# Performance work log

Hardware: AMD Instinct MI355X
Metric: run time of the kernel (lower is better)

Reference implementation:

```python
import jax, jax.numpy as jnp
import numpy as np

N = 8192
CUTOFF_LOWER = 0.0
CUTOFF_UPPER = 5.0
MAX_PAIRS = 64 * N  # max_num_pairs = -64 -> 64 neighbors per atom
BOX_L = 45.0


def setup_inputs() -> dict:
    key = jax.random.key(0)
    k1, _ = jax.random.split(key)
    pos = jax.random.uniform(k1, (N, 3), dtype=jnp.float32) * BOX_L
    batch = jnp.zeros((N,), dtype=jnp.int32)
    return {"pos": pos, "batch": batch}


def reference(pos, batch):
    # Brute O(N^2) neighbor search, cutoff_lower <= r < cutoff_upper,
    # loop=False (no self pairs), include_transpose=True (both (i,j) and (j,i)),
    # resize_to_fit=False: fixed-size output padded with (-1,-1) pairs.
    n = pos.shape[0]
    diff = pos[:, None, :] - pos[None, :, :]          # [N, N, 3] edge_vec = pos_i - pos_j
    d2 = jnp.sum(diff * diff, axis=-1)                 # [N, N]
    same_batch = batch[:, None] == batch[None, :]
    not_self = ~jnp.eye(n, dtype=bool)
    mask = same_batch & not_self & (d2 < CUTOFF_UPPER ** 2) & (d2 >= CUTOFF_LOWER ** 2)
    flat = mask.reshape(-1)
    count = jnp.sum(flat)
    # static-size compaction (jit-compatible): first MAX_PAIRS hits in row-major order
    idx = jnp.nonzero(flat, size=MAX_PAIRS, fill_value=0)[0]
    valid = jnp.arange(MAX_PAIRS) < jnp.minimum(count, MAX_PAIRS)
    i = idx // n
    j = idx % n
    edge_vec = jnp.where(valid[:, None], diff.reshape(n * n, 3)[idx], 0.0)
    d2_g = d2.reshape(-1)[idx]
    edge_weight = jnp.where(valid, jnp.sqrt(jnp.where(valid, d2_g, 1.0)), 0.0)
    edge_index = jnp.stack([jnp.where(valid, i, -1), jnp.where(valid, j, -1)], axis=0)
    edge_index = edge_index.astype(jnp.int64) if jax.config.jax_enable_x64 else edge_index.astype(jnp.int32)
    return edge_index, edge_weight, edge_vec
```

## Files before the change

### kernel.cpp

```cpp
#include <hip/hip_runtime.h>

#define NATOMS 8192
#define MAXP (64 * NATOMS)
#define R2CUT 25.0f

constexpr int ROWW = 128;
constexpr int NC1 = 9;
constexpr int NCELL = NC1 * NC1 * NC1;

__device__ __forceinline__ float d2_exact(float dx, float dy, float dz) {
    return __fadd_rn(__fadd_rn(__fmul_rn(dx, dx), __fmul_rn(dy, dy)),
                     __fmul_rn(dz, dz));
}

__device__ __forceinline__ int cellOf(float v) {
    int c = (int)((double)v * 0.2);
    return c < 0 ? 0 : (c > NC1 - 1 ? NC1 - 1 : c);
}

__global__ __launch_bounds__(256) void nl_init(float4* __restrict__ out) {
    const int total4 = 6 * MAXP / 4;
    const int neg4   = 2 * MAXP / 4;
    const float4 negv  = make_float4(-1.f, -1.f, -1.f, -1.f);
    const float4 zerov = make_float4(0.f, 0.f, 0.f, 0.f);
    int idx = blockIdx.x * blockDim.x + threadIdx.x;
    int stride = gridDim.x * blockDim.x;
    for (int k = idx; k < total4; k += stride)
        out[k] = (k < neg4) ? negv : zerov;
}

__global__ __launch_bounds__(1024) void bin_all(const float* __restrict__ pos,
                                                int* __restrict__ cellStart,
                                                int* __restrict__ sortedIdx,
                                                float4* __restrict__ sortedPos) {
    __shared__ unsigned int hist[NCELL];
    __shared__ unsigned int scanbuf[1024];
    __shared__ unsigned int starts[NCELL + 1];
    const int t = threadIdx.x;
    if (t < NCELL) hist[t] = 0u;
    __syncthreads();
    int myCell[8], mySlot[8];
#pragma unroll
    for (int k = 0; k < 8; ++k) {
        const int a = t + k * 1024;
        const float x = pos[3 * a], y = pos[3 * a + 1], z = pos[3 * a + 2];
        const int c = (cellOf(z) * NC1 + cellOf(y)) * NC1 + cellOf(x);
        myCell[k] = c;
        mySlot[k] = (int)atomicAdd(&hist[c], 1u);
    }
    __syncthreads();
    const unsigned int v = (t < NCELL) ? hist[t] : 0u;
    scanbuf[t] = v;
    __syncthreads();
    for (int off = 1; off < 1024; off <<= 1) {
        const unsigned int u = (t >= off) ? scanbuf[t - off] : 0u;
        __syncthreads();
        scanbuf[t] += u;
        __syncthreads();
    }
    const unsigned int ex = scanbuf[t] - v;
    if (t < NCELL) { starts[t] = ex; cellStart[t] = (int)ex; }
    if (t == 0)    { starts[NCELL] = NATOMS; cellStart[NCELL] = NATOMS; }
    __syncthreads();
#pragma unroll
    for (int k = 0; k < 8; ++k) {
        const int a = t + k * 1024;
        const int p = (int)starts[myCell[k]] + mySlot[k];
        sortedIdx[p] = a;
        sortedPos[p] = make_float4(pos[3 * a], pos[3 * a + 1], pos[3 * a + 2], 0.f);
    }
}

__global__ __launch_bounds__(512) void nl_neigh(const float* __restrict__ pos,
                                                const int* __restrict__ batch,
                                                const int* __restrict__ cellStart,
                                                const int* __restrict__ sortedIdx,
                                                const float4* __restrict__ sortedPos,
                                                unsigned short* __restrict__ rowbuf,
                                                int* __restrict__ counts) {
    __shared__ unsigned int bm[8][256];
    const int tid = threadIdx.x;
    const int lane = tid & 63;
    const int wave = tid >> 6;
    const int i = blockIdx.x * 8 + wave;
    unsigned int* sb = bm[wave];
    sb[lane] = 0u; sb[lane + 64] = 0u; sb[lane + 128] = 0u; sb[lane + 192] = 0u;

    const float xi = pos[3 * i], yi = pos[3 * i + 1], zi = pos[3 * i + 2];
    const int bi = batch[i];
    const int cx = cellOf(xi), cy = cellOf(yi), cz = cellOf(zi);
    const int xlo = cx > 0 ? cx - 1 : 0;
    const int xhi = cx < NC1 - 1 ? cx + 1 : NC1 - 1;

    for (int dz = -1; dz <= 1; ++dz) {
        const int czz = cz + dz;
        if ((unsigned)czz > (unsigned)(NC1 - 1)) continue;
        for (int dy = -1; dy <= 1; ++dy) {
            const int cyy = cy + dy;
            if ((unsigned)cyy > (unsigned)(NC1 - 1)) continue;
            const int base = (czz * NC1 + cyy) * NC1;
            const int s = cellStart[base + xlo];
            const int e = cellStart[base + xhi + 1];
            for (int k = s + lane; k < e; k += 64) {
                const float4 p = sortedPos[k];
                const int j = sortedIdx[k];
                const float dxv = xi - p.x;
                const float dyv = yi - p.y;
                const float dzv = zi - p.z;
                const float d2 = d2_exact(dxv, dyv, dzv);
                if (d2 < R2CUT && j != i && batch[j] == bi)
                    atomicOr(&sb[j >> 5], 1u << (j & 31));
            }
        }
    }

    unsigned short* rb = rowbuf + (size_t)i * ROWW;
    int total = 0;
#pragma unroll
    for (int g = 0; g < 4; ++g) {
        unsigned int w = sb[g * 64 + lane];
        const int c = __popc(w);
        int incl = c;
        for (int off = 1; off < 64; off <<= 1) {
            const int u = __shfl_up(incl, off);
            if (lane >= off) incl += u;
        }
        int o = total + incl - c;
        const unsigned int jbase = (unsigned)(g * 64 + lane) * 32u;
        while (w) {
            const int b = __ffs(w) - 1;
            w &= w - 1u;
            if (o < ROWW) rb[o] = (unsigned short)(jbase + (unsigned)b);
            ++o;
        }
        total += __shfl(incl, 63);
    }
    if (lane == 0) counts[i] = total > ROWW ? ROWW : total;
}

__global__ __launch_bounds__(256) void nl_scan(const int* __restrict__ counts,
                                               int* __restrict__ offsets) {
    __shared__ int ssum[256];
    const int tid = threadIdx.x;
    const int base = tid * 32;
    int c[32];
    int s = 0;
#pragma unroll
    for (int k = 0; k < 32; ++k) { c[k] = counts[base + k]; s += c[k]; }
    ssum[tid] = s;
    __syncthreads();
    for (int off = 1; off < 256; off <<= 1) {
        const int v = (tid >= off) ? ssum[tid - off] : 0;
        __syncthreads();
        ssum[tid] += v;
        __syncthreads();
    }
    int run = ssum[tid] - s;
#pragma unroll
    for (int k = 0; k < 32; ++k) { offsets[base + k] = run; run += c[k]; }
}

__global__ __launch_bounds__(512) void nl_scatter(const float* __restrict__ pos,
                                                  const unsigned short* __restrict__ rowbuf,
                                                  const int* __restrict__ counts,
                                                  const int* __restrict__ offsets,
                                                  float* __restrict__ out) {
    const int tid = threadIdx.x;
    const int lane = tid & 63;
    const int wave = tid >> 6;
    const int i = blockIdx.x * 8 + wave;
    const int cnt = counts[i];
    const int base = offsets[i];
    const float xi = pos[3 * i], yi = pos[3 * i + 1], zi = pos[3 * i + 2];
    const float fi = (float)i;
    const unsigned short* rb = rowbuf + (size_t)i * ROWW;
    float* __restrict__ outI = out;
    float* __restrict__ outJ = out + MAXP;
    float* __restrict__ outW = out + 2 * MAXP;
    float* __restrict__ outV = out + 3 * MAXP;
    for (int k = lane; k < cnt; k += 64) {
        const int j = rb[k];
        const float dxv = xi - pos[3 * j];
        const float dyv = yi - pos[3 * j + 1];
        const float dzv = zi - pos[3 * j + 2];
        const float d2 = d2_exact(dxv, dyv, dzv);
        const int slot = base + k;
        if (slot < MAXP) {
            outI[slot] = fi;
            outJ[slot] = (float)j;
            outW[slot] = sqrtf(d2);
            outV[3 * slot + 0] = dxv;
            outV[3 * slot + 1] = dyv;
            outV[3 * slot + 2] = dzv;
        }
    }
}

extern "C" void kernel_launch(void* const* d_in, const int* in_sizes, int n_in,
                              void* d_out, int out_size, void* d_ws, size_t ws_size,
                              hipStream_t stream) {
    const float* pos = (const float*)d_in[0];
    const int* batch = (const int*)d_in[1];
    float* out = (float*)d_out;

    char* ws = (char*)d_ws;
    int* counts           = (int*)(ws);
    int* offsets          = (int*)(ws + (32 << 10));
    int* cellStart        = (int*)(ws + (64 << 10));
    int* sortedIdx        = (int*)(ws + (68 << 10));
    float4* sortedPos     = (float4*)(ws + (100 << 10));
    unsigned short* rowbuf = (unsigned short*)(ws + (240 << 10));

    nl_init<<<2048, 256, 0, stream>>>((float4*)out);
    bin_all<<<1, 1024, 0, stream>>>(pos, cellStart, sortedIdx, sortedPos);
    nl_neigh<<<NATOMS / 8, 512, 0, stream>>>(pos, batch, cellStart, sortedIdx,
                                             sortedPos, rowbuf, counts);
    nl_scan<<<1, 256, 0, stream>>>(counts, offsets);
    nl_scatter<<<NATOMS / 8, 512, 0, stream>>>(pos, rowbuf, counts, offsets, out);
}
```

Measured before the change: 98.96 us.

## Fuse all neighbor-list stages into one cooperative kernel with grid syncs

Replaces the five separate launches (init, binning, neighbor search, scan, scatter) with one cooperative kernel of 256 blocks that uses grid.sync between phases. Binning switches from a single-block counting sort to fixed-capacity per-cell buckets filled by global atomics. Each block's row lists and offsets stay in shared memory instead of a global row buffer. This removes launch gaps, the serial single-block binning pass and global round trips, but adds grid-wide barriers, leaves only 256 blocks for the search phase, and drops atoms when a cell holds more than 48.

Result: slower. 176.7 us (+78.5%).

```diff
diff --git a/kernel.cpp b/kernel.cpp
--- a/kernel.cpp
+++ b/kernel.cpp
@@ -1,12 +1,20 @@
 #include <hip/hip_runtime.h>
+#include <hip/hip_cooperative_groups.h>
+
+namespace cg = cooperative_groups;
 
 #define NATOMS 8192
 #define MAXP (64 * NATOMS)
 #define R2CUT 25.0f
 
-constexpr int ROWW = 128;
 constexpr int NC1 = 9;
 constexpr int NCELL = NC1 * NC1 * NC1;
+constexpr int BCAP = 48;
+constexpr int ROWW = 128;
+constexpr int NBLK = 256;
+constexpr int NTHR = 512;
+constexpr int RPB = NATOMS / NBLK;
+constexpr int GTH = NBLK * NTHR;
 
 __device__ __forceinline__ float d2_exact(float dx, float dy, float dz) {
     return __fadd_rn(__fadd_rn(__fmul_rn(dx, dx), __fmul_rn(dy, dy)),
@@ -18,180 +26,171 @@
     return c < 0 ? 0 : (c > NC1 - 1 ? NC1 - 1 : c);
 }
 
-__global__ __launch_bounds__(256) void nl_init(float4* __restrict__ out) {
-    const int total4 = 6 * MAXP / 4;
-    const int neg4   = 2 * MAXP / 4;
-    const float4 negv  = make_float4(-1.f, -1.f, -1.f, -1.f);
-    const float4 zerov = make_float4(0.f, 0.f, 0.f, 0.f);
-    int idx = blockIdx.x * blockDim.x + threadIdx.x;
-    int stride = gridDim.x * blockDim.x;
-    for (int k = idx; k < total4; k += stride)
-        out[k] = (k < neg4) ? negv : zerov;
-}
-
-__global__ __launch_bounds__(1024) void bin_all(const float* __restrict__ pos,
-                                                int* __restrict__ cellStart,
-                                                int* __restrict__ sortedIdx,
-                                                float4* __restrict__ sortedPos) {
-    __shared__ unsigned int hist[NCELL];
-    __shared__ unsigned int scanbuf[1024];
-    __shared__ unsigned int starts[NCELL + 1];
+__global__ void __launch_bounds__(NTHR, 4)
+nl_all(const float* __restrict__ pos, const int* __restrict__ batch,
+       int* __restrict__ bucketCount, float4* __restrict__ buckets,
+       int* __restrict__ counts, float* __restrict__ out) {
+    cg::grid_group grid = cg::this_grid();
     const int t = threadIdx.x;
-    if (t < NCELL) hist[t] = 0u;
-    __syncthreads();
-    int myCell[8], mySlot[8];
+    const int b = blockIdx.x;
+    const int gtid = b * NTHR + t;
+    const int lane = t & 63;
+    const int wave = t >> 6;
+
+    __shared__ unsigned int bm[8][256];
+    __shared__ unsigned short rb[RPB][ROWW];
+    __shared__ int partial[NTHR];
+    __shared__ int rowoff[RPB];
+    __shared__ int rowcnt[RPB];
+
+    if (gtid < NCELL) bucketCount[gtid] = 0;
+    grid.sync();
+
+    {
+        float4* o4 = (float4*)out;
+        const float4 negv  = make_float4(-1.f, -1.f, -1.f, -1.f);
+        const float4 zerov = make_float4(0.f, 0.f, 0.f, 0.f);
+        o4[gtid]           = negv;
+        o4[gtid + GTH]     = negv;
+        o4[gtid + 2 * GTH] = zerov;
+        o4[gtid + 3 * GTH] = zerov;
+        o4[gtid + 4 * GTH] = zerov;
+        o4[gtid + 5 * GTH] = zerov;
+        if (gtid < NATOMS) {
+            const float x = pos[3 * gtid], y = pos[3 * gtid + 1],
+                        z = pos[3 * gtid + 2];
+            const int c = (cellOf(z) * NC1 + cellOf(y)) * NC1 + cellOf(x);
+            const int slot = atomicAdd(&bucketCount[c], 1);
+            if (slot < BCAP)
+                buckets[c * BCAP + slot] =
+                    make_float4(x, y, z, __int_as_float(gtid));
+        }
+    }
+    grid.sync();
+
+    for (int rr = 0; rr < 4; ++rr) {
+        const int q = wave * 4 + rr;
+        const int i = b * RPB + q;
+        unsigned int* sb = bm[wave];
+        sb[lane] = 0u; sb[lane + 64] = 0u; sb[lane + 128] = 0u; sb[lane + 192] = 0u;
+        const float xi = pos[3 * i], yi = pos[3 * i + 1], zi = pos[3 * i + 2];
+        const int bi = batch[i];
+        const int cx = cellOf(xi), cy = cellOf(yi), cz = cellOf(zi);
+        const int xlo = cx > 0 ? cx - 1 : 0;
+        const int nc = (cx < NC1 - 1 ? cx + 1 : NC1 - 1) - xlo + 1;
+        for (int dz = -1; dz <= 1; ++dz) {
+            const int czz = cz + dz;
+            if ((unsigned)czz >= (unsigned)NC1) continue;
+            for (int dy = -1; dy <= 1; ++dy) {
+                const int cyy = cy + dy;
+                if ((unsigned)cyy >= (unsigned)NC1) continue;
+                const int c0 = (czz * NC1 + cyy) * NC1 + xlo;
+                const int n0 = min(bucketCount[c0], BCAP);
+                const int n1 = nc > 1 ? min(bucketCount[c0 + 1], BCAP) : 0;
+                const int n2 = nc > 2 ? min(bucketCount[c0 + 2], BCAP) : 0;
+                const int m = n0 + n1 + n2;
+                for (int k = lane; k < m; k += 64) {
+                    int cell, idx;
+                    if (k < n0)           { cell = c0;     idx = k; }
+                    else if (k < n0 + n1) { cell = c0 + 1; idx = k - n0; }
+                    else                  { cell = c0 + 2; idx = k - n0 - n1; }
+                    const float4 p = buckets[cell * BCAP + idx];
+                    const int j = __float_as_int(p.w);
+                    const float dxv = xi - p.x;
+                    const float dyv = yi - p.y;
+                    const float dzv = zi - p.z;
+                    const float d2 = d2_exact(dxv, dyv, dzv);
+                    if (d2 < R2CUT && j != i && batch[j] == bi)
+                        atomicOr(&sb[j >> 5], 1u << (j & 31));
+                }
+            }
+        }
+        int total = 0;
 #pragma unroll
-    for (int k = 0; k < 8; ++k) {
-        const int a = t + k * 1024;
-        const float x = pos[3 * a], y = pos[3 * a + 1], z = pos[3 * a + 2];
-        const int c = (cellOf(z) * NC1 + cellOf(y)) * NC1 + cellOf(x);
-        myCell[k] = c;
-        mySlot[k] = (int)atomicAdd(&hist[c], 1u);
-    }
-    __syncthreads();
-    const unsigned int v = (t < NCELL) ? hist[t] : 0u;
-    scanbuf[t] = v;
-    __syncthreads();
-    for (int off = 1; off < 1024; off <<= 1) {
-        const unsigned int u = (t >= off) ? scanbuf[t - off] : 0u;
+        for (int g4 = 0; g4 < 4; ++g4) {
+            unsigned int w = sb[g4 * 64 + lane];
+            const int c = __popc(w);
+            int incl = c;
+            for (int off = 1; off < 64; off <<= 1) {
+                const int u = __shfl_up(incl, off);
+                if (lane >= off) incl += u;
+            }
+            int o = total + incl - c;
+            const unsigned int jbase = (unsigned)(g4 * 64 + lane) * 32u;
+            while (w) {
+                const int bit = __ffs(w) - 1;
+                w &= w - 1u;
+                if (o < ROWW) rb[q][o] = (unsigned short)(jbase + (unsigned)bit);
+                ++o;
+            }
+            total += __shfl(incl, 63);
+        }
+        if (lane == 0) {
+            const int cv = total > ROWW ? ROWW : total;
+            counts[i] = cv;
+            rowcnt[q] = cv;
+        }
+    }
+    grid.sync();
+
+    {
+        const int4* c4 = (const int4*)counts;
+        int4 v0 = c4[4 * t + 0], v1 = c4[4 * t + 1];
+        int4 v2 = c4[4 * t + 2], v3 = c4[4 * t + 3];
+        const int s = v0.x + v0.y + v0.z + v0.w + v1.x + v1.y + v1.z + v1.w +
+                      v2.x + v2.y + v2.z + v2.w + v3.x + v3.y + v3.z + v3.w;
+        partial[t] = s;
         __syncthreads();
-        scanbuf[t] += u;
+        for (int off = 1; off < NTHR; off <<= 1) {
+            const int u = (t >= off) ? partial[t - off] : 0;
+            __syncthreads();
+            partial[t] += u;
+            __syncthreads();
+        }
+        if ((t >> 1) == b) {
+            int vals[16];
+            vals[0] = v0.x;  vals[1] = v0.y;  vals[2] = v0.z;  vals[3] = v0.w;
+            vals[4] = v1.x;  vals[5] = v1.y;  vals[6] = v1.z;  vals[7] = v1.w;
+            vals[8] = v2.x;  vals[9] = v2.y;  vals[10] = v2.z; vals[11] = v2.w;
+            vals[12] = v3.x; vals[13] = v3.y; vals[14] = v3.z; vals[15] = v3.w;
+            const int qb = (t & 1) * 16;
+            int run = partial[t] - s;
+#pragma unroll
+            for (int q2 = 0; q2 < 16; ++q2) {
+                rowoff[qb + q2] = run;
+                run += vals[q2];
+            }
+        }
         __syncthreads();
     }
-    const unsigned int ex = scanbuf[t] - v;
-    if (t < NCELL) { starts[t] = ex; cellStart[t] = (int)ex; }
-    if (t == 0)    { starts[NCELL] = NATOMS; cellStart[NCELL] = NATOMS; }
-    __syncthreads();
-#pragma unroll
-    for (int k = 0; k < 8; ++k) {
-        const int a = t + k * 1024;
-        const int p = (int)starts[myCell[k]] + mySlot[k];
-        sortedIdx[p] = a;
-        sortedPos[p] = make_float4(pos[3 * a], pos[3 * a + 1], pos[3 * a + 2], 0.f);
-    }
-}
-
-__global__ __launch_bounds__(512) void nl_neigh(const float* __restrict__ pos,
-                                                const int* __restrict__ batch,
-                                                const int* __restrict__ cellStart,
-                                                const int* __restrict__ sortedIdx,
-                                                const float4* __restrict__ sortedPos,
-                                                unsigned short* __restrict__ rowbuf,
-                                                int* __restrict__ counts) {
-    __shared__ unsigned int bm[8][256];
-    const int tid = threadIdx.x;
-    const int lane = tid & 63;
-    const int wave = tid >> 6;
-    const int i = blockIdx.x * 8 + wave;
-    unsigned int* sb = bm[wave];
-    sb[lane] = 0u; sb[lane + 64] = 0u; sb[lane + 128] = 0u; sb[lane + 192] = 0u;
-
-    const float xi = pos[3 * i], yi = pos[3 * i + 1], zi = pos[3 * i + 2];
-    const int bi = batch[i];
-    const int cx = cellOf(xi), cy = cellOf(yi), cz = cellOf(zi);
-    const int xlo = cx > 0 ? cx - 1 : 0;
-    const int xhi = cx < NC1 - 1 ? cx + 1 : NC1 - 1;
-
-    for (int dz = -1; dz <= 1; ++dz) {
-        const int czz = cz + dz;
-        if ((unsigned)czz > (unsigned)(NC1 - 1)) continue;
-        for (int dy = -1; dy <= 1; ++dy) {
-            const int cyy = cy + dy;
-            if ((unsigned)cyy > (unsigned)(NC1 - 1)) continue;
-            const int base = (czz * NC1 + cyy) * NC1;
-            const int s = cellStart[base + xlo];
-            const int e = cellStart[base + xhi + 1];
-            for (int k = s + lane; k < e; k += 64) {
-                const float4 p = sortedPos[k];
-                const int j = sortedIdx[k];
-                const float dxv = xi - p.x;
-                const float dyv = yi - p.y;
-                const float dzv = zi - p.z;
+    {
+        float* __restrict__ outI = out;
+        float* __restrict__ outJ = out + MAXP;
+        float* __restrict__ outW = out + 2 * MAXP;
+        float* __restrict__ outV = out + 3 * MAXP;
+        for (int rr = 0; rr < 4; ++rr) {
+            const int q = wave * 4 + rr;
+            const int i = b * RPB + q;
+            const int cnt = rowcnt[q];
+            const int base = rowoff[q];
+            const float xi = pos[3 * i], yi = pos[3 * i + 1], zi = pos[3 * i + 2];
+            const float fi = (float)i;
+            for (int k = lane; k < cnt; k += 64) {
+                const int j = rb[q][k];
+                const float dxv = xi - pos[3 * j];
+                const float dyv = yi - pos[3 * j + 1];
+                const float dzv = zi - pos[3 * j + 2];
                 const float d2 = d2_exact(dxv, dyv, dzv);
-                if (d2 < R2CUT && j != i && batch[j] == bi)
-                    atomicOr(&sb[j >> 5], 1u << (j & 31));
-            }
-        }
-    }
-
-    unsigned short* rb = rowbuf + (size_t)i * ROWW;
-    int total = 0;
-#pragma unroll
-    for (int g = 0; g < 4; ++g) {
-        unsigned int w = sb[g * 64 + lane];
-        const int c = __popc(w);
-        int incl = c;
-        for (int off = 1; off < 64; off <<= 1) {
-            const int u = __shfl_up(incl, off);
-            if (lane >= off) incl += u;
-        }
-        int o = total + incl - c;
-        const unsigned int jbase = (unsigned)(g * 64 + lane) * 32u;
-        while (w) {
-            const int b = __ffs(w) - 1;
-            w &= w - 1u;
-            if (o < ROWW) rb[o] = (unsigned short)(jbase + (unsigned)b);
-            ++o;
-        }
-        total += __shfl(incl, 63);
-    }
-    if (lane == 0) counts[i] = total > ROWW ? ROWW : total;
-}
-
-__global__ __launch_bounds__(256) void nl_scan(const int* __restrict__ counts,
-                                               int* __restrict__ offsets) {
-    __shared__ int ssum[256];
-    const int tid = threadIdx.x;
-    const int base = tid * 32;
-    int c[32];
-    int s = 0;
-#pragma unroll
-    for (int k = 0; k < 32; ++k) { c[k] = counts[base + k]; s += c[k]; }
-    ssum[tid] = s;
-    __syncthreads();
-    for (int off = 1; off < 256; off <<= 1) {
-        const int v = (tid >= off) ? ssum[tid - off] : 0;
-        __syncthreads();
-        ssum[tid] += v;
-        __syncthreads();
-    }
-    int run = ssum[tid] - s;
-#pragma unroll
-    for (int k = 0; k < 32; ++k) { offsets[base + k] = run; run += c[k]; }
-}
-
-__global__ __launch_bounds__(512) void nl_scatter(const float* __restrict__ pos,
-                                                  const unsigned short* __restrict__ rowbuf,
-                                                  const int* __restrict__ counts,
-                                                  const int* __restrict__ offsets,
-                                                  float* __restrict__ out) {
-    const int tid = threadIdx.x;
-    const int lane = tid & 63;
-    const int wave = tid >> 6;
-    const int i = blockIdx.x * 8 + wave;
-    const int cnt = counts[i];
-    const int base = offsets[i];
-    const float xi = pos[3 * i], yi = pos[3 * i + 1], zi = pos[3 * i + 2];
-    const float fi = (float)i;
-    const unsigned short* rb = rowbuf + (size_t)i * ROWW;
-    float* __restrict__ outI = out;
-    float* __restrict__ outJ = out + MAXP;
-    float* __restrict__ outW = out + 2 * MAXP;
-    float* __restrict__ outV = out + 3 * MAXP;
-    for (int k = lane; k < cnt; k += 64) {
-        const int j = rb[k];
-        const float dxv = xi - pos[3 * j];
-        const float dyv = yi - pos[3 * j + 1];
-        const float dzv = zi - pos[3 * j + 2];
-        const float d2 = d2_exact(dxv, dyv, dzv);
-        const int slot = base + k;
-        if (slot < MAXP) {
-            outI[slot] = fi;
-            outJ[slot] = (float)j;
-            outW[slot] = sqrtf(d2);
-            outV[3 * slot + 0] = dxv;
-            outV[3 * slot + 1] = dyv;
-            outV[3 * slot + 2] = dzv;
+                const int slot = base + k;
+                if (slot < MAXP) {
+                    outI[slot] = fi;
+                    outJ[slot] = (float)j;
+                    outW[slot] = sqrtf(d2);
+                    outV[3 * slot + 0] = dxv;
+                    outV[3 * slot + 1] = dyv;
+                    outV[3 * slot + 2] = dzv;
+                }
+            }
         }
     }
 }
@@ -204,17 +203,11 @@
     float* out = (float*)d_out;
 
     char* ws = (char*)d_ws;
-    int* counts           = (int*)(ws);
-    int* offsets          = (int*)(ws + (32 << 10));
-    int* cellStart        = (int*)(ws + (64 << 10));
-    int* sortedIdx        = (int*)(ws + (68 << 10));
-    float4* sortedPos     = (float4*)(ws + (100 << 10));
-    unsigned short* rowbuf = (unsigned short*)(ws + (240 << 10));
-
-    nl_init<<<2048, 256, 0, stream>>>((float4*)out);
-    bin_all<<<1, 1024, 0, stream>>>(pos, cellStart, sortedIdx, sortedPos);
-    nl_neigh<<<NATOMS / 8, 512, 0, stream>>>(pos, batch, cellStart, sortedIdx,
-                                             sortedPos, rowbuf, counts);
-    nl_scan<<<1, 256, 0, stream>>>(counts, offsets);
-    nl_scatter<<<NATOMS / 8, 512, 0, stream>>>(pos, rowbuf, counts, offsets, out);
-}
+    int* counts       = (int*)ws;
+    int* bucketCount  = (int*)(ws + (32 << 10));
+    float4* buckets   = (float4*)(ws + (64 << 10));
+
+    void* args[] = {(void*)&pos,     (void*)&batch,  (void*)&bucketCount,
+                    (void*)&buckets, (void*)&counts, (void*)&out};
+    hipLaunchCooperativeKernel(nl_all, dim3(NBLK), dim3(NTHR), args, 0, stream);
+}
```
